# Kernel optimization log

Hardware: AMD Instinct MI355X
Metric: run time of the kernel (lower is better)

## Reference

```python
import jax, jax.numpy as jnp
import numpy as np

HIDDEN = 512
HEADS = 8
PREFIX = 1  # prefix_size: rows >= PREFIX may not attend to cols < PREFIX (except causal tril already zeroed those only partially)


def setup_inputs() -> dict:
    key = jax.random.key(0)
    k1, k2, k3 = jax.random.split(key, 3)
    B, L, D = 2, 4096, HIDDEN
    x = jax.random.normal(k1, (B, L, D), dtype=jnp.float32)
    # torch Linear(hidden, 3*hidden): y = x @ W^T + b; we store W^T directly as [D, 3D]
    w_in = jax.random.normal(k2, (D, 3 * D), dtype=jnp.float32) * (1.0 / np.sqrt(D))
    b_in = jnp.zeros((3 * D,), dtype=jnp.float32)
    w_out = jax.random.normal(k3, (D, D), dtype=jnp.float32) * (1.0 / np.sqrt(D))
    b_out = jnp.zeros((D,), dtype=jnp.float32)
    return {"x": x, "w_in": w_in, "b_in": b_in, "w_out": w_out, "b_out": b_out}


def _prefix_causal_mask(L):
    # tril(ones) then zero out [prefix:, :prefix]
    m = jnp.tril(jnp.ones((L, L), dtype=bool))
    m = m.at[PREFIX:, :PREFIX].set(False)
    return m  # True = attend allowed


def reference(x, w_in, b_in, w_out, b_out):
    B, L, D = x.shape
    H, hd = HEADS, D // HEADS
    qkv = x @ w_in + b_in  # [B, L, 3D]
    q, k, v = jnp.split(qkv, 3, axis=-1)
    q = q.reshape(B, L, H, hd).transpose(0, 2, 1, 3)  # [B,H,L,hd]
    k = k.reshape(B, L, H, hd).transpose(0, 2, 1, 3)
    v = v.reshape(B, L, H, hd).transpose(0, 2, 1, 3)
    scale = 1.0 / np.sqrt(hd).astype(np.float32)
    attn = jnp.einsum('bhqd,bhkd->bhqk', q, k) * scale  # [B,H,L,L]
    mask = _prefix_causal_mask(L)
    attn = jnp.where(mask[None, None, :, :], attn, -jnp.inf)
    attn = jax.nn.softmax(attn, axis=-1)  # dropout p=0.0 -> identity
    out = jnp.einsum('bhqk,bhkd->bhqd', attn, v)  # [B,H,L,hd]
    out = out.transpose(0, 2, 1, 3).reshape(B, L, D)
    return out @ w_out + b_out
```

## Files before the change

kernel.cpp:

```cpp
#include <hip/hip_runtime.h>
#include <hip/hip_bf16.h>

#define BSZ   2
#define LSEQ  4096
#define DH    512
#define NH    8
#define HDIM  64

typedef unsigned short ushort_t;
typedef __attribute__((ext_vector_type(8))) short s8v;
typedef __attribute__((ext_vector_type(4))) float f4v;

__device__ __forceinline__ ushort_t f2bf(float f) {
    __hip_bfloat16 h = __float2bfloat16(f);
    return *(ushort_t*)&h;
}

__device__ __forceinline__ void gld_lds16(const ushort_t* g, ushort_t* l) {
    __builtin_amdgcn_global_load_lds(
        (const __attribute__((address_space(1))) void*)g,
        (__attribute__((address_space(3))) void*)l, 16, 0, 0);
}

__device__ __forceinline__ void transpose_tile(const float* __restrict__ src,
                                               ushort_t* __restrict__ dst,
                                               int R, int C, int bx, int by)
{
    __shared__ float tile[32][33];
    int r0 = by * 32, c0 = bx * 32;
    int t = threadIdx.x;
    int tr = t >> 5, tc = t & 31;
    #pragma unroll
    for (int i = 0; i < 4; i++)
        tile[tr + 8 * i][tc] = src[(size_t)(r0 + tr + 8 * i) * C + c0 + tc];
    __syncthreads();
    #pragma unroll
    for (int i = 0; i < 4; i++) {
        int oc = tr + 8 * i;
        dst[(size_t)(c0 + oc) * R + r0 + tc] = f2bf(tile[tc][oc]);
    }
}

__global__ __launch_bounds__(256) void prep(const float* __restrict__ x,
                                            ushort_t* __restrict__ xb,
                                            const float* __restrict__ w_in,
                                            ushort_t* __restrict__ w_inT,
                                            const float* __restrict__ w_out,
                                            ushort_t* __restrict__ w_outT)
{
    int bx = blockIdx.x;
    if (bx < 4096) {
        int i = (bx * 256 + threadIdx.x) * 4;
        float4 v = *(const float4*)&x[i];
        ushort_t o[4] = {f2bf(v.x), f2bf(v.y), f2bf(v.z), f2bf(v.w)};
        *(uint2*)&xb[i] = *(uint2*)o;
    } else if (bx < 4864) {
        int idx = bx - 4096;
        transpose_tile(w_in, w_inT, DH, 3 * DH, idx % 48, idx / 48);
    } else {
        int idx = bx - 4864;
        transpose_tile(w_out, w_outT, DH, DH, idx % 16, idx / 16);
    }
}

__global__ __launch_bounds__(256) void vtrans(const ushort_t* __restrict__ qkv,
                                              ushort_t* __restrict__ vt)
{
    __shared__ ushort_t T[64][72];
    const int lt = blockIdx.x, h = blockIdx.y, b = blockIdx.z;
    const int l0 = lt * 64;
    const int t = threadIdx.x;
    {
        int r = t >> 2, c = (t & 3) * 16;
        size_t g = ((size_t)(b * LSEQ + l0 + r)) * (3 * DH) + 2 * DH + h * HDIM + c;
        *(uint4*)&T[r][c]     = *(const uint4*)&qkv[g];
        *(uint4*)&T[r][c + 8] = *(const uint4*)&qkv[g + 8];
    }
    __syncthreads();
    {
        int d = t >> 2, cl = (t & 3) * 16;
        ushort_t tmp[16];
        #pragma unroll
        for (int j = 0; j < 16; j++) tmp[j] = T[cl + j][d];
        size_t g = ((size_t)((b * NH + h) * 64 + d)) * LSEQ + l0 + cl;
        *(uint4*)&vt[g]     = *(uint4*)&tmp[0];
        *(uint4*)&vt[g + 8] = *(uint4*)&tmp[8];
    }
}

template <typename OUT>
__global__ __launch_bounds__(256) void gemm_bt(const ushort_t* __restrict__ A,
                                               const ushort_t* __restrict__ Bt,
                                               const float* __restrict__ bias,
                                               OUT* __restrict__ C,
                                               int M, int N, int K)
{
    __shared__ ushort_t As[128 * 32];
    __shared__ ushort_t Bs[128 * 32];
    const int tid = threadIdx.x;
    const int row0 = blockIdx.y * 128, col0 = blockIdx.x * 128;
    const int wid = tid >> 6, lane = tid & 63;
    const int wm = wid >> 1, wn = wid & 1;
    const int quad = lane >> 4, ln = lane & 15;

    f4v acc[4][4] = {};

    const int srow = (lane >> 2);
    const int scol = (lane & 3) * 8;

    for (int k0 = 0; k0 < K; k0 += 32) {
        #pragma unroll
        for (int t = 0; t < 2; t++) {
            int chunk = wid * 2 + t;
            int r = chunk * 16 + srow;
            gld_lds16(&A[(size_t)(row0 + r) * K + k0 + scol], &As[chunk * 512]);
            gld_lds16(&Bt[(size_t)(col0 + r) * K + k0 + scol], &Bs[chunk * 512]);
        }
        __syncthreads();
        s8v af[4], bf[4];
        #pragma unroll
        for (int mt = 0; mt < 4; mt++)
            af[mt] = *(const s8v*)&As[(wm * 64 + mt * 16 + ln) * 32 + quad * 8];
        #pragma unroll
        for (int nt = 0; nt < 4; nt++)
            bf[nt] = *(const s8v*)&Bs[(wn * 64 + nt * 16 + ln) * 32 + quad * 8];
        #pragma unroll
        for (int mt = 0; mt < 4; mt++)
            #pragma unroll
            for (int nt = 0; nt < 4; nt++)
                acc[mt][nt] = __builtin_amdgcn_mfma_f32_16x16x32_bf16(
                    af[mt], bf[nt], acc[mt][nt], 0, 0, 0);
        __syncthreads();
    }

    #pragma unroll
    for (int mt = 0; mt < 4; mt++) {
        #pragma unroll
        for (int nt = 0; nt < 4; nt++) {
            int c = col0 + wn * 64 + nt * 16 + ln;
            float bv = bias[c];
            #pragma unroll
            for (int reg = 0; reg < 4; reg++) {
                int r = row0 + wm * 64 + mt * 16 + quad * 4 + reg;
                float v = acc[mt][nt][reg] + bv;
                if constexpr (sizeof(OUT) == 2)
                    C[(size_t)r * N + c] = (OUT)f2bf(v);
                else
                    C[(size_t)r * N + c] = v;
            }
        }
    }
}

__global__ __launch_bounds__(128) void flash_mfma(const ushort_t* __restrict__ qkv,
                                                  const ushort_t* __restrict__ vt,
                                                  ushort_t* __restrict__ att)
{
    __shared__ ushort_t Ks[64 * 72];
    __shared__ ushort_t Vs[64 * 72];
    __shared__ ushort_t Ps[64 * 72];

    const int p = blockIdx.x;
    const int h = blockIdx.y, b = blockIdx.z;
    const int tid = threadIdx.x;
    const int w = tid >> 6, lane = tid & 63;
    const int quad = lane >> 4, ln = lane & 15;

    const int sr = tid >> 1, sc = (tid & 1) * 32;
    const int ldsw = sr * 72 + sc;
    const size_t kstep = (size_t)64 * 3 * DH;
    const float C_EXP = 0.18033688011112042f;

    const int qts[2] = {63 - p, p};

    for (int ti = 0; ti < 2; ti++) {
        const int qt = qts[ti], q0 = qt * 64;
        const int qrow0 = q0 + w * 32;

        s8v qa[2][2];
        #pragma unroll
        for (int qg = 0; qg < 2; qg++) {
            const ushort_t* qrow = qkv
                + ((size_t)(b * LSEQ + qrow0 + qg * 16 + ln)) * (3 * DH) + h * HDIM;
            qa[qg][0] = *(const s8v*)(qrow + quad * 8);
            qa[qg][1] = *(const s8v*)(qrow + 32 + quad * 8);
        }

        float l_s[2] = {0.0f, 0.0f};
        f4v o_acc[2][4] = {};

        size_t gk = ((size_t)(b * LSEQ + sr)) * (3 * DH) + DH + h * HDIM + sc;
        size_t gv = ((size_t)((b * NH + h) * 64 + sr)) * LSEQ + sc;
        uint4 pk0 = *(const uint4*)&qkv[gk];
        uint4 pk1 = *(const uint4*)&qkv[gk + 8];
        uint4 pk2 = *(const uint4*)&qkv[gk + 16];
        uint4 pk3 = *(const uint4*)&qkv[gk + 24];
        uint4 pv0 = *(const uint4*)&vt[gv];
        uint4 pv1 = *(const uint4*)&vt[gv + 8];
        uint4 pv2 = *(const uint4*)&vt[gv + 16];
        uint4 pv3 = *(const uint4*)&vt[gv + 24];

        for (int kt = 0; kt <= qt; kt++) {
            const int k0 = kt * 64;
            __syncthreads();
            *(uint4*)&Ks[ldsw]      = pk0;
            *(uint4*)&Ks[ldsw + 8]  = pk1;
            *(uint4*)&Ks[ldsw + 16] = pk2;
            *(uint4*)&Ks[ldsw + 24] = pk3;
            *(uint4*)&Vs[ldsw]      = pv0;
            *(uint4*)&Vs[ldsw + 8]  = pv1;
            *(uint4*)&Vs[ldsw + 16] = pv2;
            *(uint4*)&Vs[ldsw + 24] = pv3;
            if (kt < qt) {
                gk += kstep; gv += 64;
                pk0 = *(const uint4*)&qkv[gk];
                pk1 = *(const uint4*)&qkv[gk + 8];
                pk2 = *(const uint4*)&qkv[gk + 16];
                pk3 = *(const uint4*)&qkv[gk + 24];
                pv0 = *(const uint4*)&vt[gv];
                pv1 = *(const uint4*)&vt[gv + 8];
                pv2 = *(const uint4*)&vt[gv + 16];
                pv3 = *(const uint4*)&vt[gv + 24];
            }
            __syncthreads();

            s8v kb[4][2], vb[4][2];
            #pragma unroll
            for (int nt = 0; nt < 4; nt++) {
                kb[nt][0] = *(const s8v*)&Ks[(nt * 16 + ln) * 72 + quad * 8];
                kb[nt][1] = *(const s8v*)&Ks[(nt * 16 + ln) * 72 + 32 + quad * 8];
            }
            #pragma unroll
            for (int dt = 0; dt < 4; dt++) {
                vb[dt][0] = *(const s8v*)&Vs[(dt * 16 + ln) * 72 + quad * 8];
                vb[dt][1] = *(const s8v*)&Vs[(dt * 16 + ln) * 72 + 32 + quad * 8];
            }

            #pragma unroll
            for (int qg = 0; qg < 2; qg++) {
                f4v s[4] = {};
                #pragma unroll
                for (int nt = 0; nt < 4; nt++) {
                    s[nt] = __builtin_amdgcn_mfma_f32_16x16x32_bf16(kb[nt][0], qa[qg][0], s[nt], 0, 0, 0);
                    s[nt] = __builtin_amdgcn_mfma_f32_16x16x32_bf16(kb[nt][1], qa[qg][1], s[nt], 0, 0, 0);
                }

                float pp[4][4];
                const int q = qrow0 + qg * 16 + ln;
                if (kt == qt) {
                    #pragma unroll
                    for (int nt = 0; nt < 4; nt++) {
                        #pragma unroll
                        for (int reg = 0; reg < 4; reg++) {
                            int kidx = k0 + nt * 16 + quad * 4 + reg;
                            bool valid = (kidx <= q) && (kidx >= 1 || q == 0);
                            pp[nt][reg] = valid ? __builtin_amdgcn_exp2f(s[nt][reg] * C_EXP) : 0.0f;
                        }
                    }
                } else {
                    #pragma unroll
                    for (int nt = 0; nt < 4; nt++)
                        #pragma unroll
                        for (int reg = 0; reg < 4; reg++)
                            pp[nt][reg] = __builtin_amdgcn_exp2f(s[nt][reg] * C_EXP);
                    if (kt == 0 && quad == 0)
                        pp[0][0] = 0.0f;
                }

                #pragma unroll
                for (int nt = 0; nt < 4; nt++)
                    l_s[qg] += (pp[nt][0] + pp[nt][1]) + (pp[nt][2] + pp[nt][3]);

                const int prow = (w * 32 + qg * 16 + ln) * 72;
                #pragma unroll
                for (int nt = 0; nt < 4; nt++) {
                    unsigned int lo = (unsigned int)f2bf(pp[nt][0]) | ((unsigned int)f2bf(pp[nt][1]) << 16);
                    unsigned int hi = (unsigned int)f2bf(pp[nt][2]) | ((unsigned int)f2bf(pp[nt][3]) << 16);
                    uint2 pkd; pkd.x = lo; pkd.y = hi;
                    *(uint2*)&Ps[prow + nt * 16 + quad * 4] = pkd;
                }

                s8v pa0 = *(const s8v*)&Ps[prow + quad * 8];
                s8v pa1 = *(const s8v*)&Ps[prow + 32 + quad * 8];
                #pragma unroll
                for (int dt = 0; dt < 4; dt++) {
                    o_acc[qg][dt] = __builtin_amdgcn_mfma_f32_16x16x32_bf16(pa0, vb[dt][0], o_acc[qg][dt], 0, 0, 0);
                    o_acc[qg][dt] = __builtin_amdgcn_mfma_f32_16x16x32_bf16(pa1, vb[dt][1], o_acc[qg][dt], 0, 0, 0);
                }
            }
        }

        #pragma unroll
        for (int qg = 0; qg < 2; qg++) {
            float lf = l_s[qg];
            lf += __shfl_xor(lf, 16);
            lf += __shfl_xor(lf, 32);
            #pragma unroll
            for (int reg = 0; reg < 4; reg++) {
                float linv = 1.0f / __shfl(lf, quad * 4 + reg);
                size_t r = (size_t)(b * LSEQ + qrow0 + qg * 16 + quad * 4 + reg);
                #pragma unroll
                for (int dt = 0; dt < 4; dt++)
                    att[r * DH + h * HDIM + dt * 16 + ln] = f2bf(o_acc[qg][dt][reg] * linv);
            }
        }
    }
}

extern "C" void kernel_launch(void* const* d_in, const int* in_sizes, int n_in,
                              void* d_out, int out_size, void* d_ws, size_t ws_size,
                              hipStream_t stream)
{
    const float* x     = (const float*)d_in[0];
    const float* w_in  = (const float*)d_in[1];
    const float* b_in  = (const float*)d_in[2];
    const float* w_out = (const float*)d_in[3];
    const float* b_out = (const float*)d_in[4];
    float* out = (float*)d_out;

    const int M = BSZ * LSEQ;
    char* ws = (char*)d_ws;
    ushort_t* xb    = (ushort_t*)ws;                       ws += (size_t)M * DH * 2;
    ushort_t* w_inT = (ushort_t*)ws;                       ws += (size_t)3 * DH * DH * 2;
    ushort_t* w_outT= (ushort_t*)ws;                       ws += (size_t)DH * DH * 2;
    ushort_t* qkvb  = (ushort_t*)ws;                       ws += (size_t)M * 3 * DH * 2;
    ushort_t* vtb   = (ushort_t*)ws;                       ws += (size_t)M * DH * 2;
    ushort_t* attb  = (ushort_t*)ws;

    prep<<<5120, 256, 0, stream>>>(x, xb, w_in, w_inT, w_out, w_outT);

    gemm_bt<ushort_t><<<dim3(3 * DH / 128, M / 128), 256, 0, stream>>>(
        xb, w_inT, b_in, qkvb, M, 3 * DH, DH);

    vtrans<<<dim3(LSEQ / 64, NH, BSZ), 256, 0, stream>>>(qkvb, vtb);

    flash_mfma<<<dim3(32, NH, BSZ), 128, 0, stream>>>(qkvb, vtb, attb);

    gemm_bt<float><<<dim3(DH / 128, M / 128), 256, 0, stream>>>(
        attb, w_outT, b_out, out, M, DH, DH);
}
```

Before: 211.3 us.

## Split key range of flash attention across two blocks with atomic fp32 accumulation

Each query-tile pair's key loop is split into two halves handled by separate blocks, doubling the flash attention grid. Partial unnormalized outputs and row sums are atomically added into zeroed fp32 buffers, and a new normalize kernel divides and converts them to bf16. The aim is better CU occupancy on a grid that was small relative to the device. The cost is extra zeroing, atomic traffic, a 16MB fp32 round trip and one more launch. Combining partials by plain addition only works because the kernel appears to use a fixed exponent offset rather than a running max.

```diff
diff --git a/kernel.cpp b/kernel.cpp
--- a/kernel.cpp
+++ b/kernel.cpp
@@ -46,7 +46,9 @@
                                             const float* __restrict__ w_in,
                                             ushort_t* __restrict__ w_inT,
                                             const float* __restrict__ w_out,
-                                            ushort_t* __restrict__ w_outT)
+                                            ushort_t* __restrict__ w_outT,
+                                            float* __restrict__ Oacc,
+                                            float* __restrict__ lacc)
 {
     int bx = blockIdx.x;
     if (bx < 4096) {
@@ -57,9 +59,17 @@
     } else if (bx < 4864) {
         int idx = bx - 4096;
         transpose_tile(w_in, w_inT, DH, 3 * DH, idx % 48, idx / 48);
-    } else {
+    } else if (bx < 5120) {
         int idx = bx - 4864;
         transpose_tile(w_out, w_outT, DH, DH, idx % 16, idx / 16);
+    } else if (bx < 9216) {
+        int i = ((bx - 5120) * 256 + threadIdx.x) * 4;
+        float4 z = {0.f, 0.f, 0.f, 0.f};
+        *(float4*)&Oacc[i] = z;
+    } else {
+        int i = ((bx - 9216) * 256 + threadIdx.x) * 4;
+        float4 z = {0.f, 0.f, 0.f, 0.f};
+        *(float4*)&lacc[i] = z;
     }
 }
 
@@ -154,13 +164,15 @@
 
 __global__ __launch_bounds__(128) void flash_mfma(const ushort_t* __restrict__ qkv,
                                                   const ushort_t* __restrict__ vt,
-                                                  ushort_t* __restrict__ att)
+                                                  float* __restrict__ Oacc,
+                                                  float* __restrict__ lacc)
 {
     __shared__ ushort_t Ks[64 * 72];
     __shared__ ushort_t Vs[64 * 72];
     __shared__ ushort_t Ps[64 * 72];
 
-    const int p = blockIdx.x;
+    const int p     = blockIdx.x >> 1;
+    const int khalf = blockIdx.x & 1;
     const int h = blockIdx.y, b = blockIdx.z;
     const int tid = threadIdx.x;
     const int w = tid >> 6, lane = tid & 63;
@@ -176,6 +188,9 @@
     for (int ti = 0; ti < 2; ti++) {
         const int qt = qts[ti], q0 = qt * 64;
         const int qrow0 = q0 + w * 32;
+        const int n = qt + 1;
+        const int ktBeg = khalf ? ((n + 1) >> 1) : 0;
+        const int ktEnd = khalf ? n : ((n + 1) >> 1);
 
         s8v qa[2][2];
         #pragma unroll
@@ -189,8 +204,8 @@
         float l_s[2] = {0.0f, 0.0f};
         f4v o_acc[2][4] = {};
 
-        size_t gk = ((size_t)(b * LSEQ + sr)) * (3 * DH) + DH + h * HDIM + sc;
-        size_t gv = ((size_t)((b * NH + h) * 64 + sr)) * LSEQ + sc;
+        size_t gk = ((size_t)(b * LSEQ + ktBeg * 64 + sr)) * (3 * DH) + DH + h * HDIM + sc;
+        size_t gv = ((size_t)((b * NH + h) * 64 + sr)) * LSEQ + ktBeg * 64 + sc;
         uint4 pk0 = *(const uint4*)&qkv[gk];
         uint4 pk1 = *(const uint4*)&qkv[gk + 8];
         uint4 pk2 = *(const uint4*)&qkv[gk + 16];
@@ -200,7 +215,7 @@
         uint4 pv2 = *(const uint4*)&vt[gv + 16];
         uint4 pv3 = *(const uint4*)&vt[gv + 24];
 
-        for (int kt = 0; kt <= qt; kt++) {
+        for (int kt = ktBeg; kt < ktEnd; kt++) {
             const int k0 = kt * 64;
             __syncthreads();
             *(uint4*)&Ks[ldsw]      = pk0;
@@ -211,7 +226,7 @@
             *(uint4*)&Vs[ldsw + 8]  = pv1;
             *(uint4*)&Vs[ldsw + 16] = pv2;
             *(uint4*)&Vs[ldsw + 24] = pv3;
-            if (kt < qt) {
+            if (kt + 1 < ktEnd) {
                 gk += kstep; gv += 64;
                 pk0 = *(const uint4*)&qkv[gk];
                 pk1 = *(const uint4*)&qkv[gk + 8];
@@ -295,16 +310,36 @@
             float lf = l_s[qg];
             lf += __shfl_xor(lf, 16);
             lf += __shfl_xor(lf, 32);
-            #pragma unroll
-            for (int reg = 0; reg < 4; reg++) {
-                float linv = 1.0f / __shfl(lf, quad * 4 + reg);
-                size_t r = (size_t)(b * LSEQ + qrow0 + qg * 16 + quad * 4 + reg);
-                #pragma unroll
-                for (int dt = 0; dt < 4; dt++)
-                    att[r * DH + h * HDIM + dt * 16 + ln] = f2bf(o_acc[qg][dt][reg] * linv);
-            }
-        }
-    }
+            if (quad == 0)
+                atomicAdd(&lacc[((size_t)(b * NH + h)) * LSEQ + qrow0 + qg * 16 + ln], lf);
+            #pragma unroll
+            for (int dt = 0; dt < 4; dt++)
+                #pragma unroll
+                for (int reg = 0; reg < 4; reg++)
+                    atomicAdd(&Oacc[((size_t)(b * LSEQ + qrow0 + qg * 16 + quad * 4 + reg)) * DH
+                                    + h * HDIM + dt * 16 + ln],
+                              o_acc[qg][dt][reg]);
+        }
+    }
+}
+
+__global__ __launch_bounds__(256) void normalize(const float* __restrict__ Oacc,
+                                                 const float* __restrict__ lacc,
+                                                 ushort_t* __restrict__ att)
+{
+    int t = blockIdx.x * 256 + threadIdx.x;
+    int row = t >> 5;
+    int col0 = (t & 31) * 16;
+    int h = col0 >> 6;
+    int b = row >> 12, l = row & (LSEQ - 1);
+    float linv = 1.0f / lacc[((size_t)(b * NH + h)) * LSEQ + l];
+    const float* o = &Oacc[(size_t)row * DH + col0];
+    ushort_t tmp[16];
+    #pragma unroll
+    for (int j = 0; j < 16; j++) tmp[j] = f2bf(o[j] * linv);
+    size_t g = (size_t)row * DH + col0;
+    *(uint4*)&att[g]     = *(uint4*)&tmp[0];
+    *(uint4*)&att[g + 8] = *(uint4*)&tmp[8];
 }
 
 extern "C" void kernel_launch(void* const* d_in, const int* in_sizes, int n_in,
@@ -325,16 +360,20 @@
     ushort_t* w_outT= (ushort_t*)ws;                       ws += (size_t)DH * DH * 2;
     ushort_t* qkvb  = (ushort_t*)ws;                       ws += (size_t)M * 3 * DH * 2;
     ushort_t* vtb   = (ushort_t*)ws;                       ws += (size_t)M * DH * 2;
-    ushort_t* attb  = (ushort_t*)ws;
-
-    prep<<<5120, 256, 0, stream>>>(x, xb, w_in, w_inT, w_out, w_outT);
+    ushort_t* attb  = (ushort_t*)ws;                       ws += (size_t)M * DH * 2;
+    float*    Oacc  = (float*)ws;                          ws += (size_t)M * DH * 4;
+    float*    lacc  = (float*)ws;
+
+    prep<<<9280, 256, 0, stream>>>(x, xb, w_in, w_inT, w_out, w_outT, Oacc, lacc);
 
     gemm_bt<ushort_t><<<dim3(3 * DH / 128, M / 128), 256, 0, stream>>>(
         xb, w_inT, b_in, qkvb, M, 3 * DH, DH);
 
     vtrans<<<dim3(LSEQ / 64, NH, BSZ), 256, 0, stream>>>(qkvb, vtb);
 
-    flash_mfma<<<dim3(32, NH, BSZ), 128, 0, stream>>>(qkvb, vtb, attb);
+    flash_mfma<<<dim3(64, NH, BSZ), 128, 0, stream>>>(qkvb, vtb, Oacc, lacc);
+
+    normalize<<<1024, 256, 0, stream>>>(Oacc, lacc, attb);
 
     gemm_bt<float><<<dim3(DH / 128, M / 128), 256, 0, stream>>>(
         attb, w_outT, b_out, out, M, DH, DH);
```

Result: faster. 194.6 us (-7.9%).
